# Kernel tuning notes

Hardware: AMD Instinct MI355X
Metric: run time of the kernel (lower is better)

The kernel has to match this reference:

```python
import jax, jax.numpy as jnp
import numpy as np

N = 50000   # nodes
E = 800000  # edges
H = 128     # hidden dim
V = 50000   # feats_per_node (embedding vocab)


def setup_inputs() -> dict:
    key = jax.random.key(0)
    ks = jax.random.split(key, 16)
    s = 0.05  # keep activations in a sane range
    return {
        "node_ids": jax.random.randint(ks[0], (N,), 0, V),
        "src": jax.random.randint(ks[1], (E,), 0, N),
        "dst": jnp.sort(jax.random.randint(ks[2], (E,), 0, N)),
        "emb": jax.random.normal(ks[3], (V, H), jnp.float32) * s,
        "W_pool1": jax.random.normal(ks[4], (H, H), jnp.float32) * s,
        "b_pool1": jax.random.normal(ks[5], (H,), jnp.float32) * s,
        "W_self1": jax.random.normal(ks[6], (H, H), jnp.float32) * s,
        "W_neigh1": jax.random.normal(ks[7], (H, H), jnp.float32) * s,
        "b1": jax.random.normal(ks[8], (H,), jnp.float32) * s,
        "W_pool2": jax.random.normal(ks[9], (H, H), jnp.float32) * s,
        "b_pool2": jax.random.normal(ks[10], (H,), jnp.float32) * s,
        "W_self2": jax.random.normal(ks[11], (H, H), jnp.float32) * s,
        "W_neigh2": jax.random.normal(ks[12], (H, H), jnp.float32) * s,
        "b2": jax.random.normal(ks[13], (H,), jnp.float32) * s,
    }


def _sage_pool_layer(h, src, dst, W_pool, b_pool, W_self, W_neigh, b):
    # DGL SAGEConv('pool'): per-src MLP, gather over edges, segmented max per dst.
    m = jax.nn.relu(h @ W_pool + b_pool)              # [N, H]
    msgs = m[src]                                     # [E, H] gather
    agg = jax.ops.segment_max(msgs, dst, num_segments=N,
                              indices_are_sorted=True)  # [N, H]
    agg = jnp.where(jnp.isneginf(agg), 0.0, agg)      # zero-in-degree -> 0 (DGL semantics)
    return h @ W_self + agg @ W_neigh + b


def reference(node_ids, src, dst, emb,
              W_pool1, b_pool1, W_self1, W_neigh1, b1,
              W_pool2, b_pool2, W_self2, W_neigh2, b2):
    h = emb[node_ids]                                 # embedding_h on 1-hot indices
    h = _sage_pool_layer(h, src, dst, W_pool1, b_pool1, W_self1, W_neigh1, b1)
    h = _sage_pool_layer(h, src, dst, W_pool2, b_pool2, W_self2, W_neigh2, b2)
    return h
```

## Files before the change

### kernel.cpp

```cpp
#include <hip/hip_runtime.h>

#define HD 128

typedef __attribute__((ext_vector_type(8))) short short8;
typedef __attribute__((ext_vector_type(4))) float floatx4;

typedef unsigned short ushort_t;
typedef unsigned int uint_t;

__device__ __forceinline__ ushort_t f2b(float f) {
    union { float f; uint_t u; } v; v.f = f;
    uint_t r = v.u + 0x7fff + ((v.u >> 16) & 1);
    return (ushort_t)(r >> 16);
}
__device__ __forceinline__ float b_lo(uint_t p) {
    union { uint_t u; float f; } v; v.u = p << 16; return v.f;
}
__device__ __forceinline__ float b_hi(uint_t p) {
    union { uint_t u; float f; } v; v.u = p & 0xffff0000u; return v.f;
}
__device__ __forceinline__ uint_t packb(float a, float b) {
    union { float f; uint_t u; } x, y; x.f = a; y.f = b;
    return (x.u >> 16) | (y.u & 0xffff0000u);
}

__global__ __launch_bounds__(256) void k_prep(const int* __restrict__ dst, int E,
                                              int* __restrict__ rp, int N,
                                              const int* __restrict__ ids,
                                              const float* __restrict__ emb,
                                              ushort_t* __restrict__ h0,
                                              const float* W0, const float* W1,
                                              const float* W2, const float* W3,
                                              const float* W4, const float* W5,
                                              ushort_t* __restrict__ Wpk,
                                              int nbG, int nbR) {
    int b = blockIdx.x;
    if (b < nbG) {
        int idx = b * 256 + threadIdx.x;
        int row = idx >> 5;
        if (row >= N) return;
        int c = (idx & 31) * 4;
        float4 v = *(const float4*)&emb[(size_t)ids[row] * HD + c];
        uint2 o;
        o.x = (uint_t)f2b(v.x) | ((uint_t)f2b(v.y) << 16);
        o.y = (uint_t)f2b(v.z) | ((uint_t)f2b(v.w) << 16);
        *(uint2*)&h0[(size_t)row * HD + c] = o;
    } else if (b < nbG + nbR) {
        int i = (b - nbG) * 256 + threadIdx.x;
        if (i > N) return;
        int lo = 0, hi = E;
        while (lo < hi) {
            int mid = (lo + hi) >> 1;
            if (dst[mid] < i) lo = mid + 1; else hi = mid;
        }
        rp[i] = lo;
    } else {
        int bb = b - nbG - nbR;
        const float* Ws[6] = {W0, W1, W2, W3, W4, W5};
        int mat = bb >> 6;
        int o = ((bb & 63) << 8) + threadIdx.x;
        int j = o & 7, l = (o >> 3) & 63, s = (o >> 9) & 3, t = o >> 11;
        int k = s * 32 + ((l >> 4) & 3) * 8 + j;
        int n = t * 16 + (l & 15);
        Wpk[(size_t)mat * 16384 + o] = f2b(Ws[mat][k * HD + n]);
    }
}

__global__ __launch_bounds__(256) void k_pool_mfma(const ushort_t* __restrict__ h,
                                                   const ushort_t* __restrict__ Wpk,
                                                   const float* __restrict__ bias,
                                                   ushort_t* __restrict__ m, int N) {
    int wave = blockIdx.x * 4 + (threadIdx.x >> 6);
    int row0 = wave * 32;
    if (row0 >= N) return;
    int l = threadIdx.x & 63;
    int ar0 = row0 + (l & 15); if (ar0 >= N) ar0 = N - 1;
    int ar1 = ar0 + 16;        if (ar1 >= N) ar1 = N - 1;
    int ac = (l >> 4) * 8;
    short8 a0[4], a1[4];
#pragma unroll
    for (int s = 0; s < 4; ++s) {
        a0[s] = *(const short8*)&h[(size_t)ar0 * HD + s * 32 + ac];
        a1[s] = *(const short8*)&h[(size_t)ar1 * HD + s * 32 + ac];
    }
    int rb = row0 + (l >> 4) * 4;
#pragma unroll
    for (int t = 0; t < 8; ++t) {
        floatx4 acc0 = {0.f, 0.f, 0.f, 0.f};
        floatx4 acc1 = {0.f, 0.f, 0.f, 0.f};
#pragma unroll
        for (int s = 0; s < 4; ++s) {
            short8 b = *(const short8*)&Wpk[(t * 4 + s) * 512 + l * 8];
            acc0 = __builtin_amdgcn_mfma_f32_16x16x32_bf16(a0[s], b, acc0, 0, 0, 0);
            acc1 = __builtin_amdgcn_mfma_f32_16x16x32_bf16(a1[s], b, acc1, 0, 0, 0);
        }
        int col = t * 16 + (l & 15);
        float bv = bias[col];
#pragma unroll
        for (int r = 0; r < 4; ++r) {
            int g0 = rb + r, g1 = rb + 16 + r;
            if (g0 < N) m[(size_t)g0 * HD + col] = f2b(fmaxf(acc0[r] + bv, 0.f));
            if (g1 < N) m[(size_t)g1 * HD + col] = f2b(fmaxf(acc1[r] + bv, 0.f));
        }
    }
}

template <bool F32OUT>
__global__ __launch_bounds__(256) void k_dual_mfma(const ushort_t* __restrict__ h,
                                                   const ushort_t* __restrict__ agg,
                                                   const ushort_t* __restrict__ WsPk,
                                                   const ushort_t* __restrict__ WnPk,
                                                   const float* __restrict__ bias,
                                                   void* __restrict__ outp, int N) {
    int wave = blockIdx.x * 4 + (threadIdx.x >> 6);
    int row0 = wave * 32;
    if (row0 >= N) return;
    int l = threadIdx.x & 63;
    int ar0 = row0 + (l & 15); if (ar0 >= N) ar0 = N - 1;
    int ar1 = ar0 + 16;        if (ar1 >= N) ar1 = N - 1;
    int ac = (l >> 4) * 8;
    short8 ah0[4], ah1[4], ag0[4], ag1[4];
#pragma unroll
    for (int s = 0; s < 4; ++s) {
        ah0[s] = *(const short8*)&h[(size_t)ar0 * HD + s * 32 + ac];
        ah1[s] = *(const short8*)&h[(size_t)ar1 * HD + s * 32 + ac];
        ag0[s] = *(const short8*)&agg[(size_t)ar0 * HD + s * 32 + ac];
        ag1[s] = *(const short8*)&agg[(size_t)ar1 * HD + s * 32 + ac];
    }
    int rb = row0 + (l >> 4) * 4;
#pragma unroll
    for (int t = 0; t < 8; ++t) {
        floatx4 acc0 = {0.f, 0.f, 0.f, 0.f};
        floatx4 acc1 = {0.f, 0.f, 0.f, 0.f};
#pragma unroll
        for (int s = 0; s < 4; ++s) {
            short8 bs = *(const short8*)&WsPk[(t * 4 + s) * 512 + l * 8];
            acc0 = __builtin_amdgcn_mfma_f32_16x16x32_bf16(ah0[s], bs, acc0, 0, 0, 0);
            acc1 = __builtin_amdgcn_mfma_f32_16x16x32_bf16(ah1[s], bs, acc1, 0, 0, 0);
        }
#pragma unroll
        for (int s = 0; s < 4; ++s) {
            short8 bn = *(const short8*)&WnPk[(t * 4 + s) * 512 + l * 8];
            acc0 = __builtin_amdgcn_mfma_f32_16x16x32_bf16(ag0[s], bn, acc0, 0, 0, 0);
            acc1 = __builtin_amdgcn_mfma_f32_16x16x32_bf16(ag1[s], bn, acc1, 0, 0, 0);
        }
        int col = t * 16 + (l & 15);
        float bv = bias[col];
#pragma unroll
        for (int r = 0; r < 4; ++r) {
            int g0 = rb + r, g1 = rb + 16 + r;
            float v0 = acc0[r] + bv, v1 = acc1[r] + bv;
            if (F32OUT) {
                if (g0 < N) ((float*)outp)[(size_t)g0 * HD + col] = v0;
                if (g1 < N) ((float*)outp)[(size_t)g1 * HD + col] = v1;
            } else {
                if (g0 < N) ((ushort_t*)outp)[(size_t)g0 * HD + col] = f2b(v0);
                if (g1 < N) ((ushort_t*)outp)[(size_t)g1 * HD + col] = f2b(v1);
            }
        }
    }
}

__global__ __launch_bounds__(256) void k_segmax(const ushort_t* __restrict__ m,
                                                const int* __restrict__ src,
                                                const int* __restrict__ rp,
                                                ushort_t* __restrict__ agg, int N) {
    int node = blockIdx.x * 8 + (threadIdx.x >> 5);
    if (node >= N) return;
    int lane = threadIdx.x & 31;
    int beg = rp[node], end = rp[node + 1];
    float a0 = 0.f, a1 = 0.f, a2 = 0.f, a3 = 0.f;
    float c0 = 0.f, c1 = 0.f, c2 = 0.f, c3 = 0.f;
    int e = beg;
    int e4 = beg + ((end - beg) & ~3);
    for (; e < e4; e += 4) {
        int s0 = src[e], s1 = src[e + 1], s2 = src[e + 2], s3 = src[e + 3];
        uint2 p0 = *(const uint2*)&m[(size_t)s0 * HD + lane * 4];
        uint2 p1 = *(const uint2*)&m[(size_t)s1 * HD + lane * 4];
        uint2 p2 = *(const uint2*)&m[(size_t)s2 * HD + lane * 4];
        uint2 p3 = *(const uint2*)&m[(size_t)s3 * HD + lane * 4];
        a0 = fmaxf(a0, b_lo(p0.x)); a1 = fmaxf(a1, b_hi(p0.x));
        a2 = fmaxf(a2, b_lo(p0.y)); a3 = fmaxf(a3, b_hi(p0.y));
        c0 = fmaxf(c0, b_lo(p1.x)); c1 = fmaxf(c1, b_hi(p1.x));
        c2 = fmaxf(c2, b_lo(p1.y)); c3 = fmaxf(c3, b_hi(p1.y));
        a0 = fmaxf(a0, b_lo(p2.x)); a1 = fmaxf(a1, b_hi(p2.x));
        a2 = fmaxf(a2, b_lo(p2.y)); a3 = fmaxf(a3, b_hi(p2.y));
        c0 = fmaxf(c0, b_lo(p3.x)); c1 = fmaxf(c1, b_hi(p3.x));
        c2 = fmaxf(c2, b_lo(p3.y)); c3 = fmaxf(c3, b_hi(p3.y));
    }
    for (; e < end; ++e) {
        uint2 p = *(const uint2*)&m[(size_t)src[e] * HD + lane * 4];
        a0 = fmaxf(a0, b_lo(p.x)); a1 = fmaxf(a1, b_hi(p.x));
        a2 = fmaxf(a2, b_lo(p.y)); a3 = fmaxf(a3, b_hi(p.y));
    }
    a0 = fmaxf(a0, c0); a1 = fmaxf(a1, c1); a2 = fmaxf(a2, c2); a3 = fmaxf(a3, c3);
    uint2 o; o.x = packb(a0, a1); o.y = packb(a2, a3);
    *(uint2*)&agg[(size_t)node * HD + lane * 4] = o;
}

extern "C" void kernel_launch(void* const* d_in, const int* in_sizes, int n_in,
                              void* d_out, int out_size, void* d_ws, size_t ws_size,
                              hipStream_t stream) {
    const int*   node_ids = (const int*)d_in[0];
    const int*   src      = (const int*)d_in[1];
    const int*   dst      = (const int*)d_in[2];
    const float* emb      = (const float*)d_in[3];
    const float* Wp1      = (const float*)d_in[4];
    const float* bp1      = (const float*)d_in[5];
    const float* Ws1      = (const float*)d_in[6];
    const float* Wn1      = (const float*)d_in[7];
    const float* b1       = (const float*)d_in[8];
    const float* Wp2      = (const float*)d_in[9];
    const float* bp2      = (const float*)d_in[10];
    const float* Ws2      = (const float*)d_in[11];
    const float* Wn2      = (const float*)d_in[12];
    const float* b2       = (const float*)d_in[13];
    float* out = (float*)d_out;

    const int N = in_sizes[0];
    const int E = in_sizes[1];

    char* ws = (char*)d_ws;
    int* rp = (int*)ws;
    size_t off = (((size_t)(N + 1) * 4) + 255) & ~(size_t)255;
    ushort_t* Wpk  = (ushort_t*)(ws + off);
    ushort_t* h0   = Wpk + 6 * 16384;
    ushort_t* bufM = h0 + (size_t)N * HD;
    ushort_t* bufA = bufM + (size_t)N * HD;
    ushort_t* h1   = bufA + (size_t)N * HD;

    const int nbG = (N * 32 + 255) / 256;
    const int nbR = (N + 1 + 255) / 256;
    const int nbP = 6 * 64;
    const int nb_gemm = (N + 127) / 128;
    const int nb_seg  = (N + 7) / 8;

    k_prep<<<nbG + nbR + nbP, 256, 0, stream>>>(dst, E, rp, N, node_ids, emb, h0,
                                                Wp1, Ws1, Wn1, Wp2, Ws2, Wn2, Wpk,
                                                nbG, nbR);

    const ushort_t* Wp1k = Wpk;
    const ushort_t* Ws1k = Wpk + 16384;
    const ushort_t* Wn1k = Wpk + 2 * 16384;
    const ushort_t* Wp2k = Wpk + 3 * 16384;
    const ushort_t* Ws2k = Wpk + 4 * 16384;
    const ushort_t* Wn2k = Wpk + 5 * 16384;

    k_pool_mfma<<<nb_gemm, 256, 0, stream>>>(h0, Wp1k, bp1, bufM, N);
    k_segmax<<<nb_seg, 256, 0, stream>>>(bufM, src, rp, bufA, N);
    k_dual_mfma<false><<<nb_gemm, 256, 0, stream>>>(h0, bufA, Ws1k, Wn1k, b1, h1, N);

    k_pool_mfma<<<nb_gemm, 256, 0, stream>>>(h1, Wp2k, bp2, bufM, N);
    k_segmax<<<nb_seg, 256, 0, stream>>>(bufM, src, rp, bufA, N);
    k_dual_mfma<true><<<nb_gemm, 256, 0, stream>>>(h1, bufA, Ws2k, Wn2k, b2, out, N);
}
```

Measured before the change: 245.9 us.

## Fuse embedding gather into pool GEMM and layer-1 output into layer-2 pool

The embedding gather and bf16 conversion move into the first pool GEMM kernel, so h0 is produced without a separate pass. The layer-1 self/neighbor GEMM now stages its bf16 output tile in shared memory and feeds it straight into the layer-2 pool GEMM. This removes one kernel launch and a global re-read of h1. The segment-max loop is also unrolled from 4 to 8 edges for more loads in flight. The costs are extra shared memory (about 35KB per block), which may lower occupancy, and a block-level barrier.

```diff
diff --git a/kernel.cpp b/kernel.cpp
--- a/kernel.cpp
+++ b/kernel.cpp
@@ -1,6 +1,7 @@
 #include <hip/hip_runtime.h>
 
 #define HD 128
+#define LSTR 136
 
 typedef __attribute__((ext_vector_type(8))) short short8;
 typedef __attribute__((ext_vector_type(4))) float floatx4;
@@ -23,30 +24,23 @@
     union { float f; uint_t u; } x, y; x.f = a; y.f = b;
     return (x.u >> 16) | (y.u & 0xffff0000u);
 }
+__device__ __forceinline__ short8 cvt8(const float* __restrict__ p) {
+    float4 u = *(const float4*)p, v = *(const float4*)(p + 4);
+    short8 r;
+    r[0] = (short)f2b(u.x); r[1] = (short)f2b(u.y); r[2] = (short)f2b(u.z); r[3] = (short)f2b(u.w);
+    r[4] = (short)f2b(v.x); r[5] = (short)f2b(v.y); r[6] = (short)f2b(v.z); r[7] = (short)f2b(v.w);
+    return r;
+}
 
 __global__ __launch_bounds__(256) void k_prep(const int* __restrict__ dst, int E,
                                               int* __restrict__ rp, int N,
-                                              const int* __restrict__ ids,
-                                              const float* __restrict__ emb,
-                                              ushort_t* __restrict__ h0,
                                               const float* W0, const float* W1,
                                               const float* W2, const float* W3,
                                               const float* W4, const float* W5,
-                                              ushort_t* __restrict__ Wpk,
-                                              int nbG, int nbR) {
+                                              ushort_t* __restrict__ Wpk, int nbR) {
     int b = blockIdx.x;
-    if (b < nbG) {
-        int idx = b * 256 + threadIdx.x;
-        int row = idx >> 5;
-        if (row >= N) return;
-        int c = (idx & 31) * 4;
-        float4 v = *(const float4*)&emb[(size_t)ids[row] * HD + c];
-        uint2 o;
-        o.x = (uint_t)f2b(v.x) | ((uint_t)f2b(v.y) << 16);
-        o.y = (uint_t)f2b(v.z) | ((uint_t)f2b(v.w) << 16);
-        *(uint2*)&h0[(size_t)row * HD + c] = o;
-    } else if (b < nbG + nbR) {
-        int i = (b - nbG) * 256 + threadIdx.x;
+    if (b < nbR) {
+        int i = b * 256 + threadIdx.x;
         if (i > N) return;
         int lo = 0, hi = E;
         while (lo < hi) {
@@ -55,7 +49,7 @@
         }
         rp[i] = lo;
     } else {
-        int bb = b - nbG - nbR;
+        int bb = b - nbR;
         const float* Ws[6] = {W0, W1, W2, W3, W4, W5};
         int mat = bb >> 6;
         int o = ((bb & 63) << 8) + threadIdx.x;
@@ -66,10 +60,12 @@
     }
 }
 
-__global__ __launch_bounds__(256) void k_pool_mfma(const ushort_t* __restrict__ h,
-                                                   const ushort_t* __restrict__ Wpk,
-                                                   const float* __restrict__ bias,
-                                                   ushort_t* __restrict__ m, int N) {
+__global__ __launch_bounds__(256) void k_gather_pool(const int* __restrict__ ids,
+                                                     const float* __restrict__ emb,
+                                                     const ushort_t* __restrict__ Wpk,
+                                                     const float* __restrict__ bias,
+                                                     ushort_t* __restrict__ h0,
+                                                     ushort_t* __restrict__ m, int N) {
     int wave = blockIdx.x * 4 + (threadIdx.x >> 6);
     int row0 = wave * 32;
     if (row0 >= N) return;
@@ -77,11 +73,14 @@
     int ar0 = row0 + (l & 15); if (ar0 >= N) ar0 = N - 1;
     int ar1 = ar0 + 16;        if (ar1 >= N) ar1 = N - 1;
     int ac = (l >> 4) * 8;
+    int id0 = ids[ar0], id1 = ids[ar1];
     short8 a0[4], a1[4];
 #pragma unroll
     for (int s = 0; s < 4; ++s) {
-        a0[s] = *(const short8*)&h[(size_t)ar0 * HD + s * 32 + ac];
-        a1[s] = *(const short8*)&h[(size_t)ar1 * HD + s * 32 + ac];
+        a0[s] = cvt8(&emb[(size_t)id0 * HD + s * 32 + ac]);
+        a1[s] = cvt8(&emb[(size_t)id1 * HD + s * 32 + ac]);
+        *(short8*)&h0[(size_t)ar0 * HD + s * 32 + ac] = a0[s];
+        *(short8*)&h0[(size_t)ar1 * HD + s * 32 + ac] = a1[s];
     }
     int rb = row0 + (l >> 4) * 4;
 #pragma unroll
@@ -101,62 +100,6 @@
             int g0 = rb + r, g1 = rb + 16 + r;
             if (g0 < N) m[(size_t)g0 * HD + col] = f2b(fmaxf(acc0[r] + bv, 0.f));
             if (g1 < N) m[(size_t)g1 * HD + col] = f2b(fmaxf(acc1[r] + bv, 0.f));
-        }
-    }
-}
-
-template <bool F32OUT>
-__global__ __launch_bounds__(256) void k_dual_mfma(const ushort_t* __restrict__ h,
-                                                   const ushort_t* __restrict__ agg,
-                                                   const ushort_t* __restrict__ WsPk,
-                                                   const ushort_t* __restrict__ WnPk,
-                                                   const float* __restrict__ bias,
-                                                   void* __restrict__ outp, int N) {
-    int wave = blockIdx.x * 4 + (threadIdx.x >> 6);
-    int row0 = wave * 32;
-    if (row0 >= N) return;
-    int l = threadIdx.x & 63;
-    int ar0 = row0 + (l & 15); if (ar0 >= N) ar0 = N - 1;
-    int ar1 = ar0 + 16;        if (ar1 >= N) ar1 = N - 1;
-    int ac = (l >> 4) * 8;
-    short8 ah0[4], ah1[4], ag0[4], ag1[4];
-#pragma unroll
-    for (int s = 0; s < 4; ++s) {
-        ah0[s] = *(const short8*)&h[(size_t)ar0 * HD + s * 32 + ac];
-        ah1[s] = *(const short8*)&h[(size_t)ar1 * HD + s * 32 + ac];
-        ag0[s] = *(const short8*)&agg[(size_t)ar0 * HD + s * 32 + ac];
-        ag1[s] = *(const short8*)&agg[(size_t)ar1 * HD + s * 32 + ac];
-    }
-    int rb = row0 + (l >> 4) * 4;
-#pragma unroll
-    for (int t = 0; t < 8; ++t) {
-        floatx4 acc0 = {0.f, 0.f, 0.f, 0.f};
-        floatx4 acc1 = {0.f, 0.f, 0.f, 0.f};
-#pragma unroll
-        for (int s = 0; s < 4; ++s) {
-            short8 bs = *(const short8*)&WsPk[(t * 4 + s) * 512 + l * 8];
-            acc0 = __builtin_amdgcn_mfma_f32_16x16x32_bf16(ah0[s], bs, acc0, 0, 0, 0);
-            acc1 = __builtin_amdgcn_mfma_f32_16x16x32_bf16(ah1[s], bs, acc1, 0, 0, 0);
-        }
-#pragma unroll
-        for (int s = 0; s < 4; ++s) {
-            short8 bn = *(const short8*)&WnPk[(t * 4 + s) * 512 + l * 8];
-            acc0 = __builtin_amdgcn_mfma_f32_16x16x32_bf16(ag0[s], bn, acc0, 0, 0, 0);
-            acc1 = __builtin_amdgcn_mfma_f32_16x16x32_bf16(ag1[s], bn, acc1, 0, 0, 0);
-        }
-        int col = t * 16 + (l & 15);
-        float bv = bias[col];
-#pragma unroll
-        for (int r = 0; r < 4; ++r) {
-            int g0 = rb + r, g1 = rb + 16 + r;
-            float v0 = acc0[r] + bv, v1 = acc1[r] + bv;
-            if (F32OUT) {
-                if (g0 < N) ((float*)outp)[(size_t)g0 * HD + col] = v0;
-                if (g1 < N) ((float*)outp)[(size_t)g1 * HD + col] = v1;
-            } else {
-                if (g0 < N) ((ushort_t*)outp)[(size_t)g0 * HD + col] = f2b(v0);
-                if (g1 < N) ((ushort_t*)outp)[(size_t)g1 * HD + col] = f2b(v1);
-            }
         }
     }
 }
@@ -172,13 +115,16 @@
     float a0 = 0.f, a1 = 0.f, a2 = 0.f, a3 = 0.f;
     float c0 = 0.f, c1 = 0.f, c2 = 0.f, c3 = 0.f;
     int e = beg;
-    int e4 = beg + ((end - beg) & ~3);
-    for (; e < e4; e += 4) {
-        int s0 = src[e], s1 = src[e + 1], s2 = src[e + 2], s3 = src[e + 3];
-        uint2 p0 = *(const uint2*)&m[(size_t)s0 * HD + lane * 4];
-        uint2 p1 = *(const uint2*)&m[(size_t)s1 * HD + lane * 4];
-        uint2 p2 = *(const uint2*)&m[(size_t)s2 * HD + lane * 4];
-        uint2 p3 = *(const uint2*)&m[(size_t)s3 * HD + lane * 4];
+    int e8 = beg + ((end - beg) & ~7);
+    for (; e < e8; e += 8) {
+        uint2 p0 = *(const uint2*)&m[(size_t)src[e + 0] * HD + lane * 4];
+        uint2 p1 = *(const uint2*)&m[(size_t)src[e + 1] * HD + lane * 4];
+        uint2 p2 = *(const uint2*)&m[(size_t)src[e + 2] * HD + lane * 4];
+        uint2 p3 = *(const uint2*)&m[(size_t)src[e + 3] * HD + lane * 4];
+        uint2 p4 = *(const uint2*)&m[(size_t)src[e + 4] * HD + lane * 4];
+        uint2 p5 = *(const uint2*)&m[(size_t)src[e + 5] * HD + lane * 4];
+        uint2 p6 = *(const uint2*)&m[(size_t)src[e + 6] * HD + lane * 4];
+        uint2 p7 = *(const uint2*)&m[(size_t)src[e + 7] * HD + lane * 4];
         a0 = fmaxf(a0, b_lo(p0.x)); a1 = fmaxf(a1, b_hi(p0.x));
         a2 = fmaxf(a2, b_lo(p0.y)); a3 = fmaxf(a3, b_hi(p0.y));
         c0 = fmaxf(c0, b_lo(p1.x)); c1 = fmaxf(c1, b_hi(p1.x));
@@ -187,6 +133,14 @@
         a2 = fmaxf(a2, b_lo(p2.y)); a3 = fmaxf(a3, b_hi(p2.y));
         c0 = fmaxf(c0, b_lo(p3.x)); c1 = fmaxf(c1, b_hi(p3.x));
         c2 = fmaxf(c2, b_lo(p3.y)); c3 = fmaxf(c3, b_hi(p3.y));
+        a0 = fmaxf(a0, b_lo(p4.x)); a1 = fmaxf(a1, b_hi(p4.x));
+        a2 = fmaxf(a2, b_lo(p4.y)); a3 = fmaxf(a3, b_hi(p4.y));
+        c0 = fmaxf(c0, b_lo(p5.x)); c1 = fmaxf(c1, b_hi(p5.x));
+        c2 = fmaxf(c2, b_lo(p5.y)); c3 = fmaxf(c3, b_hi(p5.y));
+        a0 = fmaxf(a0, b_lo(p6.x)); a1 = fmaxf(a1, b_hi(p6.x));
+        a2 = fmaxf(a2, b_lo(p6.y)); a3 = fmaxf(a3, b_hi(p6.y));
+        c0 = fmaxf(c0, b_lo(p7.x)); c1 = fmaxf(c1, b_hi(p7.x));
+        c2 = fmaxf(c2, b_lo(p7.y)); c3 = fmaxf(c3, b_hi(p7.y));
     }
     for (; e < end; ++e) {
         uint2 p = *(const uint2*)&m[(size_t)src[e] * HD + lane * 4];
@@ -196,6 +150,150 @@
     a0 = fmaxf(a0, c0); a1 = fmaxf(a1, c1); a2 = fmaxf(a2, c2); a3 = fmaxf(a3, c3);
     uint2 o; o.x = packb(a0, a1); o.y = packb(a2, a3);
     *(uint2*)&agg[(size_t)node * HD + lane * 4] = o;
+}
+
+__global__ __launch_bounds__(256) void k_dual_pool(const ushort_t* __restrict__ h,
+                                                   const ushort_t* __restrict__ agg,
+                                                   const ushort_t* __restrict__ WsPk,
+                                                   const ushort_t* __restrict__ WnPk,
+                                                   const float* __restrict__ b1,
+                                                   const ushort_t* __restrict__ WpPk,
+                                                   const float* __restrict__ bp,
+                                                   ushort_t* __restrict__ h1,
+                                                   ushort_t* __restrict__ m2, int N) {
+    __shared__ ushort_t ls[4 * 32 * LSTR];
+    const int tid = threadIdx.x;
+    const int widx = tid >> 6;
+    const int l = tid & 63;
+    const int row0 = (blockIdx.x * 4 + widx) * 32;
+    const bool active = row0 < N;
+    ushort_t* lt = &ls[widx * 32 * LSTR];
+    const int ac = (l >> 4) * 8;
+    const int lr = (l >> 4) * 4;
+
+    if (active) {
+        int ar0 = row0 + (l & 15); if (ar0 >= N) ar0 = N - 1;
+        int ar1 = ar0 + 16;        if (ar1 >= N) ar1 = N - 1;
+        short8 ah0[4], ah1[4], ag0[4], ag1[4];
+#pragma unroll
+        for (int s = 0; s < 4; ++s) {
+            ah0[s] = *(const short8*)&h[(size_t)ar0 * HD + s * 32 + ac];
+            ah1[s] = *(const short8*)&h[(size_t)ar1 * HD + s * 32 + ac];
+            ag0[s] = *(const short8*)&agg[(size_t)ar0 * HD + s * 32 + ac];
+            ag1[s] = *(const short8*)&agg[(size_t)ar1 * HD + s * 32 + ac];
+        }
+#pragma unroll
+        for (int t = 0; t < 8; ++t) {
+            floatx4 acc0 = {0.f, 0.f, 0.f, 0.f};
+            floatx4 acc1 = {0.f, 0.f, 0.f, 0.f};
+#pragma unroll
+            for (int s = 0; s < 4; ++s) {
+                short8 bs = *(const short8*)&WsPk[(t * 4 + s) * 512 + l * 8];
+                acc0 = __builtin_amdgcn_mfma_f32_16x16x32_bf16(ah0[s], bs, acc0, 0, 0, 0);
+                acc1 = __builtin_amdgcn_mfma_f32_16x16x32_bf16(ah1[s], bs, acc1, 0, 0, 0);
+            }
+#pragma unroll
+            for (int s = 0; s < 4; ++s) {
+                short8 bn = *(const short8*)&WnPk[(t * 4 + s) * 512 + l * 8];
+                acc0 = __builtin_amdgcn_mfma_f32_16x16x32_bf16(ag0[s], bn, acc0, 0, 0, 0);
+                acc1 = __builtin_amdgcn_mfma_f32_16x16x32_bf16(ag1[s], bn, acc1, 0, 0, 0);
+            }
+            int col = t * 16 + (l & 15);
+            float bv = b1[col];
+#pragma unroll
+            for (int r = 0; r < 4; ++r) {
+                lt[(lr + r) * LSTR + col]      = f2b(acc0[r] + bv);
+                lt[(lr + 16 + r) * LSTR + col] = f2b(acc1[r] + bv);
+            }
+        }
+    }
+    __syncthreads();
+    if (!active) return;
+
+#pragma unroll
+    for (int i = 0; i < 8; ++i) {
+        int c = l + i * 64;
+        int row = c >> 4, cc = (c & 15) * 8;
+        int gr = row0 + row;
+        if (gr < N)
+            *(short8*)&h1[(size_t)gr * HD + cc] = *(const short8*)&lt[row * LSTR + cc];
+    }
+
+    short8 pa0[4], pa1[4];
+#pragma unroll
+    for (int s = 0; s < 4; ++s) {
+        pa0[s] = *(const short8*)&lt[(l & 15) * LSTR + s * 32 + ac];
+        pa1[s] = *(const short8*)&lt[((l & 15) + 16) * LSTR + s * 32 + ac];
+    }
+    int rb = row0 + lr;
+#pragma unroll
+    for (int t = 0; t < 8; ++t) {
+        floatx4 acc0 = {0.f, 0.f, 0.f, 0.f};
+        floatx4 acc1 = {0.f, 0.f, 0.f, 0.f};
+#pragma unroll
+        for (int s = 0; s < 4; ++s) {
+            short8 b = *(const short8*)&WpPk[(t * 4 + s) * 512 + l * 8];
+            acc0 = __builtin_amdgcn_mfma_f32_16x16x32_bf16(pa0[s], b, acc0, 0, 0, 0);
+            acc1 = __builtin_amdgcn_mfma_f32_16x16x32_bf16(pa1[s], b, acc1, 0, 0, 0);
+        }
+        int col = t * 16 + (l & 15);
+        float bv = bp[col];
+#pragma unroll
+        for (int r = 0; r < 4; ++r) {
+            int g0 = rb + r, g1 = rb + 16 + r;
+            if (g0 < N) m2[(size_t)g0 * HD + col] = f2b(fmaxf(acc0[r] + bv, 0.f));
+            if (g1 < N) m2[(size_t)g1 * HD + col] = f2b(fmaxf(acc1[r] + bv, 0.f));
+        }
+    }
+}
+
+__global__ __launch_bounds__(256) void k_dual_f32(const ushort_t* __restrict__ h,
+                                                  const ushort_t* __restrict__ agg,
+                                                  const ushort_t* __restrict__ WsPk,
+                                                  const ushort_t* __restrict__ WnPk,
+                                                  const float* __restrict__ bias,
+                                                  float* __restrict__ out, int N) {
+    int wave = blockIdx.x * 4 + (threadIdx.x >> 6);
+    int row0 = wave * 32;
+    if (row0 >= N) return;
+    int l = threadIdx.x & 63;
+    int ar0 = row0 + (l & 15); if (ar0 >= N) ar0 = N - 1;
+    int ar1 = ar0 + 16;        if (ar1 >= N) ar1 = N - 1;
+    int ac = (l >> 4) * 8;
+    short8 ah0[4], ah1[4], ag0[4], ag1[4];
+#pragma unroll
+    for (int s = 0; s < 4; ++s) {
+        ah0[s] = *(const short8*)&h[(size_t)ar0 * HD + s * 32 + ac];
+        ah1[s] = *(const short8*)&h[(size_t)ar1 * HD + s * 32 + ac];
+        ag0[s] = *(const short8*)&agg[(size_t)ar0 * HD + s * 32 + ac];
+        ag1[s] = *(const short8*)&agg[(size_t)ar1 * HD + s * 32 + ac];
+    }
+    int rb = row0 + (l >> 4) * 4;
+#pragma unroll
+    for (int t = 0; t < 8; ++t) {
+        floatx4 acc0 = {0.f, 0.f, 0.f, 0.f};
+        floatx4 acc1 = {0.f, 0.f, 0.f, 0.f};
+#pragma unroll
+        for (int s = 0; s < 4; ++s) {
+            short8 bs = *(const short8*)&WsPk[(t * 4 + s) * 512 + l * 8];
+            acc0 = __builtin_amdgcn_mfma_f32_16x16x32_bf16(ah0[s], bs, acc0, 0, 0, 0);
+            acc1 = __builtin_amdgcn_mfma_f32_16x16x32_bf16(ah1[s], bs, acc1, 0, 0, 0);
+        }
+#pragma unroll
+        for (int s = 0; s < 4; ++s) {
+            short8 bn = *(const short8*)&WnPk[(t * 4 + s) * 512 + l * 8];
+            acc0 = __builtin_amdgcn_mfma_f32_16x16x32_bf16(ag0[s], bn, acc0, 0, 0, 0);
+            acc1 = __builtin_amdgcn_mfma_f32_16x16x32_bf16(ag1[s], bn, acc1, 0, 0, 0);
+        }
+        int col = t * 16 + (l & 15);
+        float bv = bias[col];
+#pragma unroll
+        for (int r = 0; r < 4; ++r) {
+            int g0 = rb + r, g1 = rb + 16 + r;
+            if (g0 < N) out[(size_t)g0 * HD + col] = acc0[r] + bv;
+            if (g1 < N) out[(size_t)g1 * HD + col] = acc1[r] + bv;
+        }
+    }
 }
 
 extern "C" void kernel_launch(void* const* d_in, const int* in_sizes, int n_in,
@@ -225,19 +323,17 @@
     size_t off = (((size_t)(N + 1) * 4) + 255) & ~(size_t)255;
     ushort_t* Wpk  = (ushort_t*)(ws + off);
     ushort_t* h0   = Wpk + 6 * 16384;
-    ushort_t* bufM = h0 + (size_t)N * HD;
+    ushort_t* h1   = h0 + (size_t)N * HD;
+    ushort_t* bufM = h1 + (size_t)N * HD;
     ushort_t* bufA = bufM + (size_t)N * HD;
-    ushort_t* h1   = bufA + (size_t)N * HD;
-
-    const int nbG = (N * 32 + 255) / 256;
+
     const int nbR = (N + 1 + 255) / 256;
     const int nbP = 6 * 64;
     const int nb_gemm = (N + 127) / 128;
     const int nb_seg  = (N + 7) / 8;
 
-    k_prep<<<nbG + nbR + nbP, 256, 0, stream>>>(dst, E, rp, N, node_ids, emb, h0,
-                                                Wp1, Ws1, Wn1, Wp2, Ws2, Wn2, Wpk,
-                                                nbG, nbR);
+    k_prep<<<nbR + nbP, 256, 0, stream>>>(dst, E, rp, N,
+                                          Wp1, Ws1, Wn1, Wp2, Ws2, Wn2, Wpk, nbR);
 
     const ushort_t* Wp1k = Wpk;
     const ushort_t* Ws1k = Wpk + 16384;
@@ -246,11 +342,10 @@
     const ushort_t* Ws2k = Wpk + 4 * 16384;
     const ushort_t* Wn2k = Wpk + 5 * 16384;
 
-    k_pool_mfma<<<nb_gemm, 256, 0, stream>>>(h0, Wp1k, bp1, bufM, N);
+    k_gather_pool<<<nb_gemm, 256, 0, stream>>>(node_ids, emb, Wp1k, bp1, h0, bufM, N);
     k_segmax<<<nb_seg, 256, 0, stream>>>(bufM, src, rp, bufA, N);
-    k_dual_mfma<false><<<nb_gemm, 256, 0, stream>>>(h0, bufA, Ws1k, Wn1k, b1, h1, N);
-
-    k_pool_mfma<<<nb_gemm, 256, 0, stream>>>(h1, Wp2k, bp2, bufM, N);
+    k_dual_pool<<<nb_gemm, 256, 0, stream>>>(h0, bufA, Ws1k, Wn1k, b1,
+                                             Wp2k, bp2, h1, bufM, N);
     k_segmax<<<nb_seg, 256, 0, stream>>>(bufM, src, rp, bufA, N);
-    k_dual_mfma<true><<<nb_gemm, 256, 0, stream>>>(h1, bufA, Ws2k, Wn2k, b2, out, N);
-}
+    k_dual_f32<<<nb_gemm, 256, 0, stream>>>(h1, bufA, Ws2k, Wn2k, b2, out, N);
+}
```

Measured after the change: 245.8 us. No clear change (-0.0%).
